# Optimization experiments

Measured on AMD Instinct MI355X. Metric: run time of the kernel, lower is better.

## Reference

```python
import jax, jax.numpy as jnp
import numpy as np

B, S, H, NH, F = 4, 1024, 1024, 16, 4096
HD = H // NH
PAD = 128  # last PAD positions are padding


def layer_norm(x, g, b, eps=1e-5):
    mu = jnp.mean(x, axis=-1, keepdims=True)
    var = jnp.mean(jnp.square(x - mu), axis=-1, keepdims=True)
    return (x - mu) * jax.lax.rsqrt(var + eps) * g + b


def setup_inputs() -> dict:
    key = jax.random.key(0)
    ks = jax.random.split(key, 10)
    sc = 0.02
    x = jax.random.normal(ks[0], (B, S, H), dtype=jnp.float32)
    attn_bias = jax.random.normal(ks[1], (B, S, S), dtype=jnp.float32)
    key_padding_mask = jnp.broadcast_to(jnp.arange(S) >= (S - PAD), (B, S))
    return {
        "x": x,
        "attn_bias": attn_bias,
        "key_padding_mask": key_padding_mask,
        "qkv_w": jax.random.normal(ks[2], (H, 3 * H), dtype=jnp.float32) * sc,
        "qkv_b": jnp.zeros((3 * H,), jnp.float32),
        "proj_w": jax.random.normal(ks[3], (H, H), dtype=jnp.float32) * sc,
        "proj_b": jnp.zeros((H,), jnp.float32),
        "ln1_g": jnp.ones((H,), jnp.float32),
        "ln1_b": jnp.zeros((H,), jnp.float32),
        "ln2_g": jnp.ones((H,), jnp.float32),
        "ln2_b": jnp.zeros((H,), jnp.float32),
        "ffn_w1": jax.random.normal(ks[4], (H, F), dtype=jnp.float32) * sc,
        "ffn_b1": jnp.zeros((F,), jnp.float32),
        "ffn_w2": jax.random.normal(ks[5], (F, H), dtype=jnp.float32) * sc,
        "ffn_b2": jnp.zeros((H,), jnp.float32),
    }


def reference(x, attn_bias, key_padding_mask, qkv_w, qkv_b, proj_w, proj_b,
              ln1_g, ln1_b, ln2_g, ln2_b, ffn_w1, ffn_b1, ffn_w2, ffn_b2):
    scale = HD ** -0.5
    qkv = (x @ qkv_w + qkv_b).reshape(B, S, 3, NH, HD)
    q, k, v = (qkv[:, :, i].transpose(0, 2, 1, 3) for i in range(3))  # [B,NH,S,HD]
    scores = jnp.einsum('bhqd,bhkd->bhqk', q, k) * scale
    scores = scores + attn_bias[:, None, :, :]
    scores = jnp.where(key_padding_mask[:, None, None, :], -jnp.inf, scores)
    attn = jax.nn.softmax(scores, axis=-1)
    out = jnp.einsum('bhqk,bhkd->bhqd', attn, v)
    out = out.transpose(0, 2, 1, 3).reshape(B, S, H)
    out = out @ proj_w + proj_b
    x = layer_norm(x + out, ln1_g, ln1_b)
    h = jax.nn.gelu(x @ ffn_w1 + ffn_b1, approximate=False)
    x = layer_norm(x + (h @ ffn_w2 + ffn_b2), ln2_g, ln2_b)
    x = jnp.where(key_padding_mask[:, :, None], 0.0, x)
    return x
```

## Files before the change

### kernel.cpp

```cpp
#include <hip/hip_runtime.h>
#include <cstdint>
#include <cstddef>

#define SEQ    1024
#define HDIM   1024
#define NHEAD  16
#define HEADD  64
#define FDIM   4096
#define BROWS  4096
#define SACT   896

typedef unsigned short u16;
typedef __bf16 bf16x8 __attribute__((ext_vector_type(8)));
typedef float  f32x4  __attribute__((ext_vector_type(4)));

__device__ __forceinline__ float bf2f(u16 u) {
    union { float f; unsigned v; } x; x.v = ((unsigned)u) << 16; return x.f;
}
__device__ __forceinline__ u16 f2bf(float f) {
    union { float f; unsigned v; } x; x.f = f;
    unsigned r = x.v + 0x7FFFu + ((x.v >> 16) & 1u);
    return (u16)(r >> 16);
}

__device__ __forceinline__ f32x4 mfma16(bf16x8 a, bf16x8 b, f32x4 c) {
    return __builtin_amdgcn_mfma_f32_16x16x32_bf16(a, b, c, 0, 0, 0);
}

__device__ __forceinline__ void gload16(const void* g, void* lds) {
    __builtin_amdgcn_global_load_lds(
        (__attribute__((address_space(1))) void*)g,
        (__attribute__((address_space(3))) void*)lds,
        16, 0, 0);
}

__global__ void cvt_bf16_kernel(const float* __restrict__ in, u16* __restrict__ out) {
    int i = blockIdx.x * 256 + threadIdx.x;
    float4 v = ((const float4*)in)[i];
    ushort4 o;
    o.x = f2bf(v.x); o.y = f2bf(v.y); o.z = f2bf(v.z); o.w = f2bf(v.w);
    ((ushort4*)out)[i] = o;
}

__global__ void wcvt_kernel(const float* __restrict__ W, u16* __restrict__ WT, int K, int N) {
    __shared__ float t[32][33];
    int n0 = blockIdx.x * 32, k0 = blockIdx.y * 32;
    int tx = threadIdx.x, ty = threadIdx.y;
    #pragma unroll
    for (int i = 0; i < 32; i += 8)
        t[ty + i][tx] = W[(size_t)(k0 + ty + i) * N + n0 + tx];
    __syncthreads();
    #pragma unroll
    for (int i = 0; i < 32; i += 8)
        WT[(size_t)(n0 + ty + i) * K + k0 + tx] = f2bf(t[tx][ty + i]);
}

__global__ void transpose_v_kernel(const u16* __restrict__ qkv, u16* __restrict__ vt) {
    __shared__ u16 t[64][65];
    int bh = blockIdx.y, b = bh >> 4, h = bh & 15;
    int s0 = blockIdx.x << 6;
    int tid = threadIdx.x;
    #pragma unroll
    for (int it = 0; it < 16; ++it) {
        int idx = tid + (it << 8);
        int r = idx >> 6, c = idx & 63;
        t[r][c] = qkv[(size_t)(b * SEQ + s0 + r) * 3072 + 2048 + h * 64 + c];
    }
    __syncthreads();
    #pragma unroll
    for (int it = 0; it < 16; ++it) {
        int idx = tid + (it << 8);
        int hd = idx >> 6, s = idx & 63;
        vt[((size_t)bh * 64 + hd) * SEQ + s0 + s] = t[s][hd];
    }
}

template<int EPI>
__global__ __launch_bounds__(256, 2)
void gemm_kernel(const u16* __restrict__ A, const u16* __restrict__ Bt,
                 const float* __restrict__ bias, const float* __restrict__ res,
                 void* __restrict__ out, int M, int N, int K)
{
    __shared__ char smem[32768];
    char* sA = smem;
    char* sB = smem + 16384;
    const int tid  = threadIdx.x;
    const int wv   = tid >> 6, ln = tid & 63;
    const int lcol = ln & 15, quad = ln >> 4;
    const int wy   = wv >> 1, wx = wv & 1;
    const int mbase = blockIdx.x << 7, nbase = blockIdx.y << 7;

    f32x4 acc[4][4];
    #pragma unroll
    for (int i = 0; i < 4; ++i)
        #pragma unroll
        for (int j = 0; j < 4; ++j)
            acc[i][j] = (f32x4){0.f, 0.f, 0.f, 0.f};

    for (int k0 = 0; k0 < K; k0 += 64) {
        __syncthreads();
        #pragma unroll
        for (int c = 0; c < 4; ++c) {
            int base = (c * 4 + wv) << 10;
            int flat = base + (ln << 4);
            int row  = flat >> 7;
            int g    = ((flat >> 4) & 7) ^ (row & 7);
            gload16(A  + (size_t)(mbase + row) * K + k0 + g * 8, sA + base);
            gload16(Bt + (size_t)(nbase + row) * K + k0 + g * 8, sB + base);
        }
        __syncthreads();
        #pragma unroll
        for (int ks = 0; ks < 2; ++ks) {
            bf16x8 af[4], bfr[4];
            #pragma unroll
            for (int t = 0; t < 4; ++t) {
                int row = (wy << 6) + (t << 4) + lcol;
                int ca  = ((ks << 2) + quad) ^ (row & 7);
                af[t] = *(const bf16x8*)(sA + row * 128 + ca * 16);
                int nrow = (wx << 6) + (t << 4) + lcol;
                int cb  = ((ks << 2) + quad) ^ (nrow & 7);
                bfr[t] = *(const bf16x8*)(sB + nrow * 128 + cb * 16);
            }
            #pragma unroll
            for (int i = 0; i < 4; ++i)
                #pragma unroll
                for (int j = 0; j < 4; ++j)
                    acc[i][j] = mfma16(af[i], bfr[j], acc[i][j]);
        }
    }

    #pragma unroll
    for (int i = 0; i < 4; ++i) {
        #pragma unroll
        for (int r = 0; r < 4; ++r) {
            int grow = mbase + (wy << 6) + (i << 4) + (quad << 2) + r;
            #pragma unroll
            for (int j = 0; j < 4; ++j) {
                int gcol = nbase + (wx << 6) + (j << 4) + lcol;
                float v = acc[i][j][r] + bias[gcol];
                if (EPI == 1 || EPI == 3) v += res[(size_t)grow * N + gcol];
                if (EPI == 2) v = 0.5f * v * (1.0f + erff(v * 0.70710678f));
                if (EPI == 0 || EPI == 2)
                    ((u16*)out)[(size_t)grow * N + gcol] = f2bf(v);
                else
                    ((float*)out)[(size_t)grow * N + gcol] = v;
            }
        }
    }
}

__global__ __launch_bounds__(256, 4)
void attn_kernel(const u16* __restrict__ qkv, const u16* __restrict__ vt,
                 const float* __restrict__ bias, u16* __restrict__ out)
{
    __shared__ char sK[8192];
    __shared__ char sV[8192];
    __shared__ char pbuf[4][2048];
    const int tid  = threadIdx.x;
    const int wid  = tid >> 6, lane = tid & 63;
    const int lcol = lane & 15, quad = lane >> 4;
    const int bh = blockIdx.y, b = bh >> 4, h = bh & 15;
    const int q0 = (blockIdx.x << 6) + (wid << 4);
    char* pb = pbuf[wid];

    const u16* qrow = qkv + (size_t)(b * SEQ + q0 + lcol) * 3072 + h * 64;
    bf16x8 qf[2];
    #pragma unroll
    for (int half = 0; half < 2; ++half) {
        union { bf16x8 v; u16 u[8]; } a;
        a.v = *(const bf16x8*)(qrow + half * 32 + quad * 8);
        #pragma unroll
        for (int j = 0; j < 8; ++j) a.u[j] = f2bf(bf2f(a.u[j]) * 0.125f);
        qf[half] = a.v;
    }

    f32x4 o[4];
    #pragma unroll
    for (int nt = 0; nt < 4; ++nt) o[nt] = (f32x4){0.f, 0.f, 0.f, 0.f};
    float mrow[4] = {-1e30f, -1e30f, -1e30f, -1e30f};
    float lrow[4] = {0.f, 0.f, 0.f, 0.f};

    const u16* khead = qkv + (size_t)b * SEQ * 3072 + 1024 + h * 64;
    const u16* vhead = vt + (size_t)bh * 64 * SEQ;

    for (int kb = 0; kb < SACT; kb += 64) {
        __syncthreads();
        #pragma unroll
        for (int i = 0; i < 2; ++i) {
            int ck  = i * 256 + tid;
            int row = ck >> 3, c = ck & 7;
            int g   = c ^ (row & 7);
            gload16(khead + (size_t)(kb + row) * 3072 + g * 8, sK + ck * 16);
            gload16(vhead + (size_t)row * SEQ + kb + g * 8,    sV + ck * 16);
        }
        __syncthreads();

        f32x4 sc[4];
        #pragma unroll
        for (int j = 0; j < 4; ++j) sc[j] = (f32x4){0.f, 0.f, 0.f, 0.f};
        #pragma unroll
        for (int ks = 0; ks < 2; ++ks)
            #pragma unroll
            for (int j = 0; j < 4; ++j) {
                int n = j * 16 + lcol;
                int c = ((ks << 2) + quad) ^ (n & 7);
                bf16x8 kf = *(const bf16x8*)(sK + n * 128 + c * 16);
                sc[j] = mfma16(qf[ks], kf, sc[j]);
            }

        const float* bp = bias + ((size_t)b * SEQ + q0 + quad * 4) * SEQ + kb;
        float p[4][4], mt[4];
        #pragma unroll
        for (int i = 0; i < 4; ++i) {
            mt[i] = -1e30f;
            #pragma unroll
            for (int j = 0; j < 4; ++j) {
                p[j][i] = sc[j][i] + bp[(size_t)i * SEQ + lcol + 16 * j];
                mt[i] = fmaxf(mt[i], p[j][i]);
            }
        }
        #pragma unroll
        for (int off = 1; off < 16; off <<= 1)
            #pragma unroll
            for (int i = 0; i < 4; ++i)
                mt[i] = fmaxf(mt[i], __shfl_xor(mt[i], off));

        float al[4], st[4];
        #pragma unroll
        for (int i = 0; i < 4; ++i) {
            float mn = fmaxf(mrow[i], mt[i]);
            al[i] = __expf(mrow[i] - mn);
            mrow[i] = mn;
            st[i] = 0.f;
            #pragma unroll
            for (int j = 0; j < 4; ++j) {
                p[j][i] = __expf(p[j][i] - mn);
                st[i] += p[j][i];
            }
        }
        #pragma unroll
        for (int off = 1; off < 16; off <<= 1)
            #pragma unroll
            for (int i = 0; i < 4; ++i)
                st[i] += __shfl_xor(st[i], off);
        #pragma unroll
        for (int i = 0; i < 4; ++i) lrow[i] = lrow[i] * al[i] + st[i];
        #pragma unroll
        for (int nt = 0; nt < 4; ++nt)
            #pragma unroll
            for (int i = 0; i < 4; ++i) o[nt][i] *= al[i];

        #pragma unroll
        for (int i = 0; i < 4; ++i) {
            int row = quad * 4 + i;
            #pragma unroll
            for (int j = 0; j < 4; ++j) {
                int col = lcol + 16 * j;
                int cch = (col >> 3) ^ (row & 7);
                *(u16*)(pb + row * 128 + cch * 16 + (col & 7) * 2) = f2bf(p[j][i]);
            }
        }

        #pragma unroll
        for (int ks = 0; ks < 2; ++ks) {
            int cp = ((ks << 2) + quad) ^ (lcol & 7);
            bf16x8 pa = *(const bf16x8*)(pb + lcol * 128 + cp * 16);
            #pragma unroll
            for (int nt = 0; nt < 4; ++nt) {
                int d = nt * 16 + lcol;
                int c = ((ks << 2) + quad) ^ (d & 7);
                bf16x8 vf = *(const bf16x8*)(sV + d * 128 + c * 16);
                o[nt] = mfma16(pa, vf, o[nt]);
            }
        }
    }

    float inv[4];
    #pragma unroll
    for (int i = 0; i < 4; ++i) inv[i] = 1.0f / lrow[i];
    #pragma unroll
    for (int nt = 0; nt < 4; ++nt)
        #pragma unroll
        for (int i = 0; i < 4; ++i)
            out[(size_t)(b * SEQ + q0 + quad * 4 + i) * HDIM + h * 64 + nt * 16 + lcol]
                = f2bf(o[nt][i] * inv[i]);
}

template<int MODE>
__global__ void ln_kernel(const float* __restrict__ y, const float* __restrict__ g,
                          const float* __restrict__ bt, float* __restrict__ of32,
                          u16* __restrict__ obf)
{
    int row = blockIdx.x;
    int tid = threadIdx.x;
    if (MODE == 1) {
        int s = row & (SEQ - 1);
        if (s >= SACT) {
            float4 z = {0.f, 0.f, 0.f, 0.f};
            ((float4*)(of32 + (size_t)row * HDIM))[tid] = z;
            return;
        }
    }
    float4 v = ((const float4*)(y + (size_t)row * HDIM))[tid];
    float s1 = v.x + v.y + v.z + v.w;
    float s2 = v.x * v.x + v.y * v.y + v.z * v.z + v.w * v.w;
    #pragma unroll
    for (int off = 32; off >= 1; off >>= 1) {
        s1 += __shfl_xor(s1, off);
        s2 += __shfl_xor(s2, off);
    }
    __shared__ float rs[8];
    int wv = tid >> 6, ln = tid & 63;
    if (ln == 0) { rs[wv] = s1; rs[4 + wv] = s2; }
    __syncthreads();
    s1 = rs[0] + rs[1] + rs[2] + rs[3];
    s2 = rs[4] + rs[5] + rs[6] + rs[7];
    float mean = s1 * (1.0f / 1024.0f);
    float var  = s2 * (1.0f / 1024.0f) - mean * mean;
    float rstd = rsqrtf(var + 1e-5f);
    float4 gg = ((const float4*)g)[tid];
    float4 bb = ((const float4*)bt)[tid];
    float4 o;
    o.x = (v.x - mean) * rstd * gg.x + bb.x;
    o.y = (v.y - mean) * rstd * gg.y + bb.y;
    o.z = (v.z - mean) * rstd * gg.z + bb.z;
    o.w = (v.w - mean) * rstd * gg.w + bb.w;
    ((float4*)(of32 + (size_t)row * HDIM))[tid] = o;
    if (MODE == 0) {
        ushort4 ob;
        ob.x = f2bf(o.x); ob.y = f2bf(o.y); ob.z = f2bf(o.z); ob.w = f2bf(o.w);
        ((ushort4*)(obf + (size_t)row * HDIM))[tid] = ob;
    }
}

extern "C" void kernel_launch(void* const* d_in, const int* in_sizes, int n_in,
                              void* d_out, int out_size, void* d_ws, size_t ws_size,
                              hipStream_t stream)
{
    const float* x      = (const float*)d_in[0];
    const float* abias  = (const float*)d_in[1];
    const float* qkv_w  = (const float*)d_in[3];
    const float* qkv_b  = (const float*)d_in[4];
    const float* proj_w = (const float*)d_in[5];
    const float* proj_b = (const float*)d_in[6];
    const float* ln1_g  = (const float*)d_in[7];
    const float* ln1_b  = (const float*)d_in[8];
    const float* ln2_g  = (const float*)d_in[9];
    const float* ln2_b  = (const float*)d_in[10];
    const float* w1     = (const float*)d_in[11];
    const float* b1     = (const float*)d_in[12];
    const float* w2     = (const float*)d_in[13];
    const float* b2     = (const float*)d_in[14];
    float* out = (float*)d_out;

    char* ws = (char*)d_ws;
    const size_t MB = 1024 * 1024;
    u16*  xb     = (u16*)(ws + 0);
    u16*  aout   = xb;
    u16*  qkvb   = (u16*)(ws + 8 * MB);
    u16*  vtb    = (u16*)(ws + 32 * MB);
    u16*  hb     = (u16*)(ws + 8 * MB);
    u16*  wqkvT  = (u16*)(ws + 40 * MB);
    u16*  wprojT = (u16*)(ws + 46 * MB);
    u16*  w1T    = (u16*)(ws + 48 * MB);
    u16*  w2T    = (u16*)(ws + 56 * MB);
    u16*  x1b    = (u16*)(ws + 64 * MB);
    float* ybuf  = (float*)(ws + 72 * MB);
    float* x1f   = (float*)(ws + 88 * MB);
    (void)in_sizes; (void)n_in; (void)out_size; (void)ws_size;

    dim3 tb32(32, 8);
    cvt_bf16_kernel<<<4096, 256, 0, stream>>>(x, xb);
    wcvt_kernel<<<dim3(3072 / 32, 1024 / 32), tb32, 0, stream>>>(qkv_w, wqkvT, 1024, 3072);
    wcvt_kernel<<<dim3(1024 / 32, 1024 / 32), tb32, 0, stream>>>(proj_w, wprojT, 1024, 1024);
    wcvt_kernel<<<dim3(4096 / 32, 1024 / 32), tb32, 0, stream>>>(w1, w1T, 1024, 4096);
    wcvt_kernel<<<dim3(1024 / 32, 4096 / 32), tb32, 0, stream>>>(w2, w2T, 4096, 1024);
    gemm_kernel<0><<<dim3(32, 24), 256, 0, stream>>>(xb, wqkvT, qkv_b, nullptr, qkvb, BROWS, 3072, 1024);
    transpose_v_kernel<<<dim3(16, 64), 256, 0, stream>>>(qkvb, vtb);
    attn_kernel<<<dim3(16, 64), 256, 0, stream>>>(qkvb, vtb, abias, aout);
    gemm_kernel<1><<<dim3(32, 8), 256, 0, stream>>>(aout, wprojT, proj_b, x, ybuf, BROWS, 1024, 1024);
    ln_kernel<0><<<4096, 256, 0, stream>>>(ybuf, ln1_g, ln1_b, x1f, x1b);
    gemm_kernel<2><<<dim3(32, 32), 256, 0, stream>>>(x1b, w1T, b1, nullptr, hb, BROWS, 4096, 1024);
    gemm_kernel<3><<<dim3(32, 8), 256, 0, stream>>>(hb, w2T, b2, x1f, ybuf, BROWS, 1024, 4096);
    ln_kernel<1><<<4096, 256, 0, stream>>>(ybuf, ln2_g, ln2_b, out, nullptr);
}
```

Baseline: 394.7 us.

## Split-K the N=1024 projection and FFN2 GEMMs, summing partials in LayerNorm

The attention projection and FFN2 GEMMs now split K in half across a third grid dimension. This doubles the block count from 256 to 512 so all CUs get more work. The second half writes raw fp32 partials to spare workspace. The LayerNorm kernels add those partials before normalizing. The cost is an extra fp32 activation buffer written and read per GEMM, and workspace regions are reused as scratch.

After: 393.4 us. Within noise of the previous version (-0.3%).

```diff
diff --git a/kernel.cpp b/kernel.cpp
--- a/kernel.cpp
+++ b/kernel.cpp
@@ -75,11 +75,12 @@
     }
 }
 
-template<int EPI>
+template<int EPI, int SPLITK>
 __global__ __launch_bounds__(256, 2)
 void gemm_kernel(const u16* __restrict__ A, const u16* __restrict__ Bt,
                  const float* __restrict__ bias, const float* __restrict__ res,
-                 void* __restrict__ out, int M, int N, int K)
+                 void* __restrict__ out, float* __restrict__ out1,
+                 int M, int N, int K)
 {
     __shared__ char smem[32768];
     char* sA = smem;
@@ -90,6 +91,9 @@
     const int wy   = wv >> 1, wx = wv & 1;
     const int mbase = blockIdx.x << 7, nbase = blockIdx.y << 7;
 
+    int kstart = 0, kend = K;
+    if (SPLITK) { int kh = K >> 1; kstart = blockIdx.z * kh; kend = kstart + kh; }
+
     f32x4 acc[4][4];
     #pragma unroll
     for (int i = 0; i < 4; ++i)
@@ -97,7 +101,7 @@
         for (int j = 0; j < 4; ++j)
             acc[i][j] = (f32x4){0.f, 0.f, 0.f, 0.f};
 
-    for (int k0 = 0; k0 < K; k0 += 64) {
+    for (int k0 = kstart; k0 < kend; k0 += 64) {
         __syncthreads();
         #pragma unroll
         for (int c = 0; c < 4; ++c) {
@@ -129,6 +133,7 @@
         }
     }
 
+    const bool partial = SPLITK && (blockIdx.z == 1);
     #pragma unroll
     for (int i = 0; i < 4; ++i) {
         #pragma unroll
@@ -137,7 +142,12 @@
             #pragma unroll
             for (int j = 0; j < 4; ++j) {
                 int gcol = nbase + (wx << 6) + (j << 4) + lcol;
-                float v = acc[i][j][r] + bias[gcol];
+                float v = acc[i][j][r];
+                if (partial) {
+                    out1[(size_t)grow * N + gcol] = v;
+                    continue;
+                }
+                v += bias[gcol];
                 if (EPI == 1 || EPI == 3) v += res[(size_t)grow * N + gcol];
                 if (EPI == 2) v = 0.5f * v * (1.0f + erff(v * 0.70710678f));
                 if (EPI == 0 || EPI == 2)
@@ -286,10 +296,10 @@
                 = f2bf(o[nt][i] * inv[i]);
 }
 
-template<int MODE>
-__global__ void ln_kernel(const float* __restrict__ y, const float* __restrict__ g,
-                          const float* __restrict__ bt, float* __restrict__ of32,
-                          u16* __restrict__ obf)
+template<int MODE, int ADD2>
+__global__ void ln_kernel(const float* __restrict__ y, const float* __restrict__ y2,
+                          const float* __restrict__ g, const float* __restrict__ bt,
+                          float* __restrict__ of32, u16* __restrict__ obf)
 {
     int row = blockIdx.x;
     int tid = threadIdx.x;
@@ -302,6 +312,10 @@
         }
     }
     float4 v = ((const float4*)(y + (size_t)row * HDIM))[tid];
+    if (ADD2) {
+        float4 w = ((const float4*)(y2 + (size_t)row * HDIM))[tid];
+        v.x += w.x; v.y += w.y; v.z += w.z; v.w += w.w;
+    }
     float s1 = v.x + v.y + v.z + v.w;
     float s2 = v.x * v.x + v.y * v.y + v.z * v.z + v.w * v.w;
     #pragma unroll
@@ -367,6 +381,8 @@
     u16*  x1b    = (u16*)(ws + 64 * MB);
     float* ybuf  = (float*)(ws + 72 * MB);
     float* x1f   = (float*)(ws + 88 * MB);
+    float* pproj = (float*)(ws + 8 * MB);
+    float* pffn2 = (float*)(ws + 40 * MB);
     (void)in_sizes; (void)n_in; (void)out_size; (void)ws_size;
 
     dim3 tb32(32, 8);
@@ -375,12 +391,12 @@
     wcvt_kernel<<<dim3(1024 / 32, 1024 / 32), tb32, 0, stream>>>(proj_w, wprojT, 1024, 1024);
     wcvt_kernel<<<dim3(4096 / 32, 1024 / 32), tb32, 0, stream>>>(w1, w1T, 1024, 4096);
     wcvt_kernel<<<dim3(1024 / 32, 4096 / 32), tb32, 0, stream>>>(w2, w2T, 4096, 1024);
-    gemm_kernel<0><<<dim3(32, 24), 256, 0, stream>>>(xb, wqkvT, qkv_b, nullptr, qkvb, BROWS, 3072, 1024);
+    gemm_kernel<0, 0><<<dim3(32, 24), 256, 0, stream>>>(xb, wqkvT, qkv_b, nullptr, qkvb, nullptr, BROWS, 3072, 1024);
     transpose_v_kernel<<<dim3(16, 64), 256, 0, stream>>>(qkvb, vtb);
     attn_kernel<<<dim3(16, 64), 256, 0, stream>>>(qkvb, vtb, abias, aout);
-    gemm_kernel<1><<<dim3(32, 8), 256, 0, stream>>>(aout, wprojT, proj_b, x, ybuf, BROWS, 1024, 1024);
-    ln_kernel<0><<<4096, 256, 0, stream>>>(ybuf, ln1_g, ln1_b, x1f, x1b);
-    gemm_kernel<2><<<dim3(32, 32), 256, 0, stream>>>(x1b, w1T, b1, nullptr, hb, BROWS, 4096, 1024);
-    gemm_kernel<3><<<dim3(32, 8), 256, 0, stream>>>(hb, w2T, b2, x1f, ybuf, BROWS, 1024, 4096);
-    ln_kernel<1><<<4096, 256, 0, stream>>>(ybuf, ln2_g, ln2_b, out, nullptr);
-}
+    gemm_kernel<1, 1><<<dim3(32, 8, 2), 256, 0, stream>>>(aout, wprojT, proj_b, x, ybuf, pproj, BROWS, 1024, 1024);
+    ln_kernel<0, 1><<<4096, 256, 0, stream>>>(ybuf, pproj, ln1_g, ln1_b, x1f, x1b);
+    gemm_kernel<2, 0><<<dim3(32, 32), 256, 0, stream>>>(x1b, w1T, b1, nullptr, hb, nullptr, BROWS, 4096, 1024);
+    gemm_kernel<3, 1><<<dim3(32, 8, 2), 256, 0, stream>>>(hb, w2T, b2, x1f, ybuf, pffn2, BROWS, 1024, 4096);
+    ln_kernel<1, 1><<<4096, 256, 0, stream>>>(ybuf, pffn2, ln2_g, ln2_b, out, nullptr);
+}
```
